# Optimization experiments

Measured on AMD Instinct MI355X. Metric: run time of the kernel, lower is better.

## Reference

```python
import jax, jax.numpy as jnp
import numpy as np

B, T, D, H, HD, FF = 1024, 128, 128, 4, 32, 512
SCALE = D ** -0.5  # NOTE: original scales by full EMBED_DIM**-0.5, not head_dim
EPS = 1e-5


def setup_inputs() -> dict:
    key = jax.random.key(0)
    ks = jax.random.split(key, 14)
    s = 0.02
    return {
        "x": jax.random.normal(ks[0], (B, T, D), dtype=jnp.float32),
        "ln1_g": jnp.ones((D,), jnp.float32),
        "ln1_b": jnp.zeros((D,), jnp.float32),
        "Wq": jax.random.normal(ks[1], (H, HD, D), jnp.float32) * s,
        "Wk": jax.random.normal(ks[2], (H, HD, D), jnp.float32) * s,
        "Wv": jax.random.normal(ks[3], (H, HD, D), jnp.float32) * s,
        "Wo": jax.random.normal(ks[4], (D, D), jnp.float32) * s,
        "bo": jnp.zeros((D,), jnp.float32),
        "ln2_g": jnp.ones((D,), jnp.float32),
        "ln2_b": jnp.zeros((D,), jnp.float32),
        "W1": jax.random.normal(ks[5], (FF, D), jnp.float32) * s,
        "b1": jnp.zeros((FF,), jnp.float32),
        "W2": jax.random.normal(ks[6], (D, FF), jnp.float32) * s,
        "b2": jnp.zeros((D,), jnp.float32),
    }


def _layer_norm(x, g, b):
    mu = jnp.mean(x, axis=-1, keepdims=True)
    var = jnp.mean(jnp.square(x - mu), axis=-1, keepdims=True)
    return (x - mu) * jax.lax.rsqrt(var + EPS) * g + b


def reference(x, ln1_g, ln1_b, Wq, Wk, Wv, Wo, bo, ln2_g, ln2_b, W1, b1, W2, b2):
    # --- attention sub-block ---
    h = _layer_norm(x, ln1_g, ln1_b)                       # [B,T,D]
    q = jnp.einsum('btd,nhd->bnth', h, Wq)                 # [B,H,T,HD]
    k = jnp.einsum('btd,nhd->bnth', h, Wk)
    v = jnp.einsum('btd,nhd->bnth', h, Wv)
    scores = jnp.einsum('bnth,bnsh->bnts', q, k) * SCALE   # [B,H,T,T]
    causal = jnp.tril(jnp.ones((T, T), dtype=bool))
    scores = jnp.where(causal, scores, -jnp.inf)
    w = jax.nn.softmax(scores, axis=-1)                    # dropout = eval identity
    attn = jnp.einsum('bnts,bnsh->bnth', w, v)             # [B,H,T,HD]
    attn = attn.transpose(0, 2, 1, 3).reshape(B, T, D)     # concat heads
    x = x + attn @ Wo.T + bo
    # --- feed-forward sub-block ---
    h2 = _layer_norm(x, ln2_g, ln2_b)
    ff = jax.nn.relu(h2 @ W1.T + b1) @ W2.T + b2
    return x + ff
```

## Files before the change

### kernel.cpp

```cpp
#include <hip/hip_runtime.h>
#include <hip/hip_bf16.h>


typedef short bf16x8 __attribute__((ext_vector_type(8)));
typedef float f32x4  __attribute__((ext_vector_type(4)));
typedef unsigned short u16;
typedef unsigned int   u32;

#define TT   128
#define DDIM 128
#define FFD  512
#define PIT  136

#define OWQ 0
#define OWK 16384
#define OWV 32768
#define OWO 49152
#define OW1 65536
#define OW2 131072
#define WTOT 196608

#define QSC 0.12751744f

#if defined(__has_builtin)
#if __has_builtin(__builtin_amdgcn_exp2f)
#define EXP2F(x) __builtin_amdgcn_exp2f(x)
#else
#define EXP2F(x) exp2f(x)
#endif
#else
#define EXP2F(x) exp2f(x)
#endif

__device__ __forceinline__ u16 f2b(float f) {
    __hip_bfloat16 h = __float2bfloat16(f);
    return __builtin_bit_cast(u16, h);
}
__device__ __forceinline__ u32 pk2(float x, float y) {
    return (u32)f2b(x) | ((u32)f2b(y) << 16);
}
__device__ __forceinline__ void st_b64(u16* p, u32 lo, u32 hi) {
    uint2 v; v.x = lo; v.y = hi;
    *reinterpret_cast<uint2*>(p) = v;
}
__device__ __forceinline__ bf16x8 ldfrag(const u16* p) {
    return __builtin_bit_cast(bf16x8, *reinterpret_cast<const uint4*>(p));
}
__device__ __forceinline__ f32x4 mfma16(bf16x8 a, bf16x8 b, f32x4 c) {
    return __builtin_amdgcn_mfma_f32_16x16x32_bf16(a, b, c, 0, 0, 0);
}

__device__ __forceinline__ void quad_collect_pk(const u32 (&pkv)[8][2],
                                                bf16x8 (&fr)[4], int lane) {
    const int srcA = (lane & 15) + ((lane & 16) << 1);
    const int srcB = srcA + 16;
    const bool hi = (lane & 32) != 0;
    #pragma unroll
    for (int g = 0; g < 4; g++) {
        u32 D00 = pkv[2*g][0],     D01 = pkv[2*g][1];
        u32 D10 = pkv[2*g + 1][0], D11 = pkv[2*g + 1][1];
        u32 a00 = (u32)__shfl((int)D00, srcA);
        u32 a10 = (u32)__shfl((int)D10, srcA);
        u32 a01 = (u32)__shfl((int)D01, srcA);
        u32 a11 = (u32)__shfl((int)D11, srcA);
        u32 b00 = (u32)__shfl((int)D00, srcB);
        u32 b10 = (u32)__shfl((int)D10, srcB);
        u32 b01 = (u32)__shfl((int)D01, srcB);
        u32 b11 = (u32)__shfl((int)D11, srcB);
        uint4 q;
        q.x = hi ? a10 : a00;
        q.y = hi ? a11 : a01;
        q.z = hi ? b10 : b00;
        q.w = hi ? b11 : b01;
        fr[g] = __builtin_bit_cast(bf16x8, q);
    }
}

__global__ __launch_bounds__(256) void wprep(
    const float* __restrict__ wq, const float* __restrict__ wk,
    const float* __restrict__ wv, const float* __restrict__ wo,
    const float* __restrict__ w1, const float* __restrict__ w2,
    u16* __restrict__ dst)
{
    int i = (blockIdx.x * 256 + threadIdx.x) * 8;
    if (i >= WTOT) return;
    const float* s; int off;
    if      (i < OWK) { s = wq; off = i - OWQ; }
    else if (i < OWV) { s = wk; off = i - OWK; }
    else if (i < OWO) { s = wv; off = i - OWV; }
    else if (i < OW1) { s = wo; off = i - OWO; }
    else if (i < OW2) { s = w1; off = i - OW1; }
    else              { s = w2; off = i - OW2; }
    float4 a = *reinterpret_cast<const float4*>(s + off);
    float4 b = *reinterpret_cast<const float4*>(s + off + 4);
    uint4 o;
    o.x = pk2(a.x, a.y); o.y = pk2(a.z, a.w);
    o.z = pk2(b.x, b.y); o.w = pk2(b.z, b.w);
    *reinterpret_cast<uint4*>(dst + i) = o;
}

__global__ __launch_bounds__(512, 2) void tblock_kernel(
    const float* __restrict__ x,
    const float* __restrict__ ln1g, const float* __restrict__ ln1b,
    const u16*  __restrict__ wbf,
    const float* __restrict__ bo,
    const float* __restrict__ ln2g, const float* __restrict__ ln2b,
    const float* __restrict__ b1,   const float* __restrict__ b2,
    float* __restrict__ out)
{
    __shared__ __align__(16) u16 sm[2 * TT * PIT];
    u16* bufK = sm;
    u16* bufV = sm + TT * PIT;

    const int b    = blockIdx.x;
    const int tid  = threadIdx.x;
    const int w    = tid >> 6;
    const int l    = tid & 63;
    const int lq   = l & 15;
    const int quad = l >> 4;
    const int trow = w * 16 + lq;
    const float* xb = x + (size_t)b * (TT * DDIM);

    const u16* wq = wbf + OWQ;
    const u16* wk = wbf + OWK;
    const u16* wv = wbf + OWV;
    const u16* wo = wbf + OWO;
    const u16* w1 = wbf + OW1;
    const u16* w2 = wbf + OW2;

    bf16x8 hf[4];
    {
        float v[32];
        float s = 0.f, s2 = 0.f;
        #pragma unroll
        for (int ks = 0; ks < 4; ks++) {
            const float* src = xb + trow * DDIM + ks * 32 + quad * 8;
            float4 u0 = *reinterpret_cast<const float4*>(src);
            float4 u1 = *reinterpret_cast<const float4*>(src + 4);
            v[ks*8+0]=u0.x; v[ks*8+1]=u0.y; v[ks*8+2]=u0.z; v[ks*8+3]=u0.w;
            v[ks*8+4]=u1.x; v[ks*8+5]=u1.y; v[ks*8+6]=u1.z; v[ks*8+7]=u1.w;
            s  += u0.x+u0.y+u0.z+u0.w + u1.x+u1.y+u1.z+u1.w;
            s2 += u0.x*u0.x+u0.y*u0.y+u0.z*u0.z+u0.w*u0.w
                + u1.x*u1.x+u1.y*u1.y+u1.z*u1.z+u1.w*u1.w;
        }
        s  += __shfl_xor(s, 16);  s2 += __shfl_xor(s2, 16);
        s  += __shfl_xor(s, 32);  s2 += __shfl_xor(s2, 32);
        float mean = s * (1.f / 128.f);
        float var  = fmaxf(s2 * (1.f / 128.f) - mean * mean, 0.f);
        float rstd = rsqrtf(var + 1e-5f);
        #pragma unroll
        for (int ks = 0; ks < 4; ks++) {
            const float* gp = ln1g + ks * 32 + quad * 8;
            const float* bp = ln1b + ks * 32 + quad * 8;
            float4 g0 = *reinterpret_cast<const float4*>(gp);
            float4 g1 = *reinterpret_cast<const float4*>(gp + 4);
            float4 c0 = *reinterpret_cast<const float4*>(bp);
            float4 c1 = *reinterpret_cast<const float4*>(bp + 4);
            float gg[8] = {g0.x,g0.y,g0.z,g0.w,g1.x,g1.y,g1.z,g1.w};
            float bb[8] = {c0.x,c0.y,c0.z,c0.w,c1.x,c1.y,c1.z,c1.w};
            #pragma unroll
            for (int j = 0; j < 8; j++)
                hf[ks][j] = (short)f2b((v[ks*8+j] - mean) * rstd * gg[j] + bb[j]);
        }
    }

    #pragma unroll
    for (int mt = 0; mt < 8; mt++) {
        f32x4 acc = {0, 0, 0, 0};
        #pragma unroll
        for (int ks = 0; ks < 4; ks++) {
            bf16x8 aw = ldfrag(wk + (mt * 16 + lq) * DDIM + ks * 32 + quad * 8);
            acc = mfma16(aw, hf[ks], acc);
        }
        st_b64(bufK + trow * PIT + mt * 16 + quad * 4,
               pk2(acc[0], acc[1]), pk2(acc[2], acc[3]));
    }
    bf16x8 qf[4];
    {
        u32 qpk[8][2];
        #pragma unroll
        for (int mt = 0; mt < 8; mt++) {
            f32x4 acc = {0, 0, 0, 0};
            #pragma unroll
            for (int ks = 0; ks < 4; ks++) {
                bf16x8 aw = ldfrag(wq + (mt * 16 + lq) * DDIM + ks * 32 + quad * 8);
                acc = mfma16(aw, hf[ks], acc);
            }
            qpk[mt][0] = pk2(acc[0] * QSC, acc[1] * QSC);
            qpk[mt][1] = pk2(acc[2] * QSC, acc[3] * QSC);
        }
        quad_collect_pk(qpk, qf, l);
    }
    #pragma unroll
    for (int mt = 0; mt < 8; mt++) {
        f32x4 acc = {0, 0, 0, 0};
        #pragma unroll
        for (int ks = 0; ks < 4; ks++) {
            bf16x8 av = ldfrag(wv + (mt * 16 + lq) * DDIM + ks * 32 + quad * 8);
            acc = mfma16(av, hf[ks], acc);
        }
        #pragma unroll
        for (int r = 0; r < 4; r++)
            bufV[(mt * 16 + quad * 4 + r) * PIT + trow] = f2b(acc[r]);
    }
    __syncthreads();

    #pragma unroll
    for (int h = 0; h < 4; h++) {
        float p[8][4];
        #pragma unroll
        for (int n = 0; n < 8; n++) {
            bf16x8 ka = ldfrag(bufK + (n * 16 + lq) * PIT + h * 32 + quad * 8);
            f32x4 s4 = mfma16(ka, qf[h], f32x4{0, 0, 0, 0});
            #pragma unroll
            for (int r = 0; r < 4; r++) p[n][r] = s4[r];
        }
        __syncthreads();
        float mx = -3.0e38f;
        #pragma unroll
        for (int n = 0; n < 8; n++) {
            #pragma unroll
            for (int r = 0; r < 4; r++) {
                int sc = n * 16 + quad * 4 + r;
                mx = (sc <= trow) ? fmaxf(mx, p[n][r]) : mx;
            }
        }
        mx = fmaxf(mx, __shfl_xor(mx, 16));
        mx = fmaxf(mx, __shfl_xor(mx, 32));
        float sum = 0.f;
        u32 ppk[8][2];
        #pragma unroll
        for (int n = 0; n < 8; n++) {
            float e0, e1, e2, e3;
            {
                int sc = n * 16 + quad * 4;
                e0 = (sc     <= trow) ? EXP2F(p[n][0] - mx) : 0.f;
                e1 = (sc + 1 <= trow) ? EXP2F(p[n][1] - mx) : 0.f;
                e2 = (sc + 2 <= trow) ? EXP2F(p[n][2] - mx) : 0.f;
                e3 = (sc + 3 <= trow) ? EXP2F(p[n][3] - mx) : 0.f;
            }
            sum += e0 + e1 + e2 + e3;
            ppk[n][0] = pk2(e0, e1);
            ppk[n][1] = pk2(e2, e3);
        }
        sum += __shfl_xor(sum, 16);
        sum += __shfl_xor(sum, 32);
        float inv = 1.f / sum;
        bf16x8 pfr[4];
        quad_collect_pk(ppk, pfr, l);
        f32x4 o0 = {0, 0, 0, 0}, o1 = {0, 0, 0, 0};
        #pragma unroll
        for (int ks = 0; ks < 4; ks++) {
            bf16x8 va0 = ldfrag(bufV + (h * 32 + lq) * PIT + ks * 32 + quad * 8);
            bf16x8 va1 = ldfrag(bufV + (h * 32 + 16 + lq) * PIT + ks * 32 + quad * 8);
            o0 = mfma16(va0, pfr[ks], o0);
            o1 = mfma16(va1, pfr[ks], o1);
        }
        #pragma unroll
        for (int r = 0; r < 4; r++) { o0[r] *= inv; o1[r] *= inv; }
        st_b64(bufK + trow * PIT + h * 32 + quad * 4,
               pk2(o0[0], o0[1]), pk2(o0[2], o0[3]));
        st_b64(bufK + trow * PIT + h * 32 + 16 + quad * 4,
               pk2(o1[0], o1[1]), pk2(o1[2], o1[3]));
    }
    __syncthreads();

    float x1res[8][4];
    {
        bf16x8 woa[4];
        #pragma unroll
        for (int ks = 0; ks < 4; ks++)
            woa[ks] = ldfrag(wo + (w * 16 + lq) * DDIM + ks * 32 + quad * 8);
        const float4 bo4 = *reinterpret_cast<const float4*>(bo + w * 16 + quad * 4);
        #pragma unroll
        for (int m = 0; m < 8; m++) {
            f32x4 acc = {0, 0, 0, 0};
            #pragma unroll
            for (int ks = 0; ks < 4; ks++) {
                bf16x8 ab = ldfrag(bufK + (m * 16 + lq) * PIT + ks * 32 + quad * 8);
                acc = mfma16(woa[ks], ab, acc);
            }
            int t = m * 16 + lq;
            const float4 xv = *reinterpret_cast<const float4*>(xb + t * DDIM + w * 16 + quad * 4);
            float v0 = acc[0] + xv.x + bo4.x;
            float v1 = acc[1] + xv.y + bo4.y;
            float v2 = acc[2] + xv.z + bo4.z;
            float v3 = acc[3] + xv.w + bo4.w;
            x1res[m][0] = v0; x1res[m][1] = v1; x1res[m][2] = v2; x1res[m][3] = v3;
            st_b64(bufV + t * PIT + w * 16 + quad * 4, pk2(v0, v1), pk2(v2, v3));
        }
    }
    __syncthreads();

    {
        const int row = tid >> 2, part = tid & 3;
        const u16* src = bufV + row * PIT + part * 32;
        float v[32];
        float s = 0.f, s2 = 0.f;
        #pragma unroll
        for (int i = 0; i < 4; i++) {
            uint4 u = *reinterpret_cast<const uint4*>(src + i * 8);
            u32 arr[4] = {u.x, u.y, u.z, u.w};
            #pragma unroll
            for (int j = 0; j < 4; j++) {
                float f0 = __uint_as_float((arr[j] & 0xffffu) << 16);
                float f1 = __uint_as_float(arr[j] & 0xffff0000u);
                v[i * 8 + 2 * j] = f0; v[i * 8 + 2 * j + 1] = f1;
                s += f0 + f1; s2 += f0 * f0 + f1 * f1;
            }
        }
        s  += __shfl_xor(s, 1);  s2 += __shfl_xor(s2, 1);
        s  += __shfl_xor(s, 2);  s2 += __shfl_xor(s2, 2);
        float mean = s * (1.f / 128.f);
        float var  = fmaxf(s2 * (1.f / 128.f) - mean * mean, 0.f);
        float rstd = rsqrtf(var + 1e-5f);
        u16* dst = bufK + row * PIT + part * 32;
        #pragma unroll
        for (int i = 0; i < 4; i++) {
            u32 o4[4];
            #pragma unroll
            for (int j = 0; j < 4; j++) {
                int c = part * 32 + i * 8 + 2 * j;
                float r0 = (v[i * 8 + 2 * j]     - mean) * rstd * ln2g[c]     + ln2b[c];
                float r1 = (v[i * 8 + 2 * j + 1] - mean) * rstd * ln2g[c + 1] + ln2b[c + 1];
                o4[j] = (u32)f2b(r0) | ((u32)f2b(r1) << 16);
            }
            uint4 pk; pk.x = o4[0]; pk.y = o4[1]; pk.z = o4[2]; pk.w = o4[3];
            *reinterpret_cast<uint4*>(dst + i * 8) = pk;
        }
    }
    __syncthreads();

    f32x4 oacc[8];
    #pragma unroll
    for (int m = 0; m < 8; m++) oacc[m] = f32x4{0, 0, 0, 0};

    #pragma unroll 1
    for (int fc = 0; fc < 4; fc++) {
        const int fbase = fc * 128;
        bf16x8 w1a[4];
        #pragma unroll
        for (int ks = 0; ks < 4; ks++)
            w1a[ks] = ldfrag(w1 + (fbase + w * 16 + lq) * DDIM + ks * 32 + quad * 8);
        const float4 b14 = *reinterpret_cast<const float4*>(b1 + fbase + w * 16 + quad * 4);
        #pragma unroll
        for (int m = 0; m < 8; m++) {
            f32x4 acc = {0, 0, 0, 0};
            #pragma unroll
            for (int ks = 0; ks < 4; ks++) {
                bf16x8 hb = ldfrag(bufK + (m * 16 + lq) * PIT + ks * 32 + quad * 8);
                acc = mfma16(w1a[ks], hb, acc);
            }
            int t = m * 16 + lq;
            float g0 = fmaxf(acc[0] + b14.x, 0.f);
            float g1 = fmaxf(acc[1] + b14.y, 0.f);
            float g2 = fmaxf(acc[2] + b14.z, 0.f);
            float g3 = fmaxf(acc[3] + b14.w, 0.f);
            st_b64(bufV + t * PIT + w * 16 + quad * 4, pk2(g0, g1), pk2(g2, g3));
        }
        __syncthreads();
        bf16x8 w2a[4];
        #pragma unroll
        for (int ks = 0; ks < 4; ks++)
            w2a[ks] = ldfrag(w2 + (w * 16 + lq) * FFD + fbase + ks * 32 + quad * 8);
        #pragma unroll
        for (int m = 0; m < 8; m++) {
            #pragma unroll
            for (int ks = 0; ks < 4; ks++) {
                bf16x8 gb = ldfrag(bufV + (m * 16 + lq) * PIT + ks * 32 + quad * 8);
                oacc[m] = mfma16(w2a[ks], gb, oacc[m]);
            }
        }
        if (fc < 3) __syncthreads();
    }

    {
        const float4 b24 = *reinterpret_cast<const float4*>(b2 + w * 16 + quad * 4);
        float* ob = out + (size_t)b * (TT * DDIM);
        #pragma unroll
        for (int m = 0; m < 8; m++) {
            int t = m * 16 + lq;
            float4 o;
            o.x = oacc[m][0] + x1res[m][0] + b24.x;
            o.y = oacc[m][1] + x1res[m][1] + b24.y;
            o.z = oacc[m][2] + x1res[m][2] + b24.z;
            o.w = oacc[m][3] + x1res[m][3] + b24.w;
            *reinterpret_cast<float4*>(ob + t * DDIM + w * 16 + quad * 4) = o;
        }
    }
}

extern "C" void kernel_launch(void* const* d_in, const int* in_sizes, int n_in,
                              void* d_out, int out_size, void* d_ws, size_t ws_size,
                              hipStream_t stream) {
    const float* x    = (const float*)d_in[0];
    const float* ln1g = (const float*)d_in[1];
    const float* ln1b = (const float*)d_in[2];
    const float* Wq   = (const float*)d_in[3];
    const float* Wk   = (const float*)d_in[4];
    const float* Wv   = (const float*)d_in[5];
    const float* Wo   = (const float*)d_in[6];
    const float* bo   = (const float*)d_in[7];
    const float* ln2g = (const float*)d_in[8];
    const float* ln2b = (const float*)d_in[9];
    const float* W1   = (const float*)d_in[10];
    const float* b1   = (const float*)d_in[11];
    const float* W2   = (const float*)d_in[12];
    const float* b2   = (const float*)d_in[13];
    float* out = (float*)d_out;
    u16* wbf = (u16*)d_ws;

    wprep<<<dim3((WTOT / 8 + 255) / 256), dim3(256), 0, stream>>>(
        Wq, Wk, Wv, Wo, W1, W2, wbf);

    const int nblocks = in_sizes[0] / (TT * DDIM);
    tblock_kernel<<<dim3(nblocks), dim3(512), 0, stream>>>(
        x, ln1g, ln1b, wbf, bo, ln2g, ln2b, b1, b2, out);
}
```

Baseline: 353.3 us.

## Keep per-row activations in registers through Wo, LN2 and FFN, dropping LDS round-trips

After attention, each wave now keeps its 16 token rows in registers. Those rows feed the output projection, the second layer norm (a cross-lane shuffle reduction) and both FFN matmuls, replacing the shared-memory staging buffers and most of the block-wide barriers. The query scale is folded into Wq during weight prep, and the head loop is no longer unrolled. In exchange, each wave reads the full Wo, W1 and W2 weight fragments from global/L2 memory instead of only its 16-row slice, and register pressure rises.

```diff
diff --git a/kernel.cpp b/kernel.cpp
--- a/kernel.cpp
+++ b/kernel.cpp
@@ -84,8 +84,8 @@
 {
     int i = (blockIdx.x * 256 + threadIdx.x) * 8;
     if (i >= WTOT) return;
-    const float* s; int off;
-    if      (i < OWK) { s = wq; off = i - OWQ; }
+    const float* s; int off; float sc = 1.0f;
+    if      (i < OWK) { s = wq; off = i - OWQ; sc = QSC; }
     else if (i < OWV) { s = wk; off = i - OWK; }
     else if (i < OWO) { s = wv; off = i - OWV; }
     else if (i < OW1) { s = wo; off = i - OWO; }
@@ -94,8 +94,8 @@
     float4 a = *reinterpret_cast<const float4*>(s + off);
     float4 b = *reinterpret_cast<const float4*>(s + off + 4);
     uint4 o;
-    o.x = pk2(a.x, a.y); o.y = pk2(a.z, a.w);
-    o.z = pk2(b.x, b.y); o.w = pk2(b.z, b.w);
+    o.x = pk2(a.x * sc, a.y * sc); o.y = pk2(a.z * sc, a.w * sc);
+    o.z = pk2(b.x * sc, b.y * sc); o.w = pk2(b.z * sc, b.w * sc);
     *reinterpret_cast<uint4*>(dst + i) = o;
 }
 
@@ -168,10 +168,8 @@
     for (int mt = 0; mt < 8; mt++) {
         f32x4 acc = {0, 0, 0, 0};
         #pragma unroll
-        for (int ks = 0; ks < 4; ks++) {
-            bf16x8 aw = ldfrag(wk + (mt * 16 + lq) * DDIM + ks * 32 + quad * 8);
-            acc = mfma16(aw, hf[ks], acc);
-        }
+        for (int ks = 0; ks < 4; ks++)
+            acc = mfma16(ldfrag(wk + (mt * 16 + lq) * DDIM + ks * 32 + quad * 8), hf[ks], acc);
         st_b64(bufK + trow * PIT + mt * 16 + quad * 4,
                pk2(acc[0], acc[1]), pk2(acc[2], acc[3]));
     }
@@ -182,12 +180,10 @@
         for (int mt = 0; mt < 8; mt++) {
             f32x4 acc = {0, 0, 0, 0};
             #pragma unroll
-            for (int ks = 0; ks < 4; ks++) {
-                bf16x8 aw = ldfrag(wq + (mt * 16 + lq) * DDIM + ks * 32 + quad * 8);
-                acc = mfma16(aw, hf[ks], acc);
-            }
-            qpk[mt][0] = pk2(acc[0] * QSC, acc[1] * QSC);
-            qpk[mt][1] = pk2(acc[2] * QSC, acc[3] * QSC);
+            for (int ks = 0; ks < 4; ks++)
+                acc = mfma16(ldfrag(wq + (mt * 16 + lq) * DDIM + ks * 32 + quad * 8), hf[ks], acc);
+            qpk[mt][0] = pk2(acc[0], acc[1]);
+            qpk[mt][1] = pk2(acc[2], acc[3]);
         }
         quad_collect_pk(qpk, qf, l);
     }
@@ -195,17 +191,16 @@
     for (int mt = 0; mt < 8; mt++) {
         f32x4 acc = {0, 0, 0, 0};
         #pragma unroll
-        for (int ks = 0; ks < 4; ks++) {
-            bf16x8 av = ldfrag(wv + (mt * 16 + lq) * DDIM + ks * 32 + quad * 8);
-            acc = mfma16(av, hf[ks], acc);
-        }
+        for (int ks = 0; ks < 4; ks++)
+            acc = mfma16(ldfrag(wv + (mt * 16 + lq) * DDIM + ks * 32 + quad * 8), hf[ks], acc);
         #pragma unroll
         for (int r = 0; r < 4; r++)
             bufV[(mt * 16 + quad * 4 + r) * PIT + trow] = f2b(acc[r]);
     }
     __syncthreads();
 
-    #pragma unroll
+    u32 apk[8][2];
+    #pragma unroll 1
     for (int h = 0; h < 4; h++) {
         float p[8][4];
         #pragma unroll
@@ -215,7 +210,6 @@
             #pragma unroll
             for (int r = 0; r < 4; r++) p[n][r] = s4[r];
         }
-        __syncthreads();
         float mx = -3.0e38f;
         #pragma unroll
         for (int n = 0; n < 8; n++) {
@@ -231,14 +225,11 @@
         u32 ppk[8][2];
         #pragma unroll
         for (int n = 0; n < 8; n++) {
-            float e0, e1, e2, e3;
-            {
-                int sc = n * 16 + quad * 4;
-                e0 = (sc     <= trow) ? EXP2F(p[n][0] - mx) : 0.f;
-                e1 = (sc + 1 <= trow) ? EXP2F(p[n][1] - mx) : 0.f;
-                e2 = (sc + 2 <= trow) ? EXP2F(p[n][2] - mx) : 0.f;
-                e3 = (sc + 3 <= trow) ? EXP2F(p[n][3] - mx) : 0.f;
-            }
+            int sc = n * 16 + quad * 4;
+            float e0 = (sc     <= trow) ? EXP2F(p[n][0] - mx) : 0.f;
+            float e1 = (sc + 1 <= trow) ? EXP2F(p[n][1] - mx) : 0.f;
+            float e2 = (sc + 2 <= trow) ? EXP2F(p[n][2] - mx) : 0.f;
+            float e3 = (sc + 3 <= trow) ? EXP2F(p[n][3] - mx) : 0.f;
             sum += e0 + e1 + e2 + e3;
             ppk[n][0] = pk2(e0, e1);
             ppk[n][1] = pk2(e2, e3);
@@ -256,136 +247,101 @@
             o0 = mfma16(va0, pfr[ks], o0);
             o1 = mfma16(va1, pfr[ks], o1);
         }
-        #pragma unroll
-        for (int r = 0; r < 4; r++) { o0[r] *= inv; o1[r] *= inv; }
-        st_b64(bufK + trow * PIT + h * 32 + quad * 4,
-               pk2(o0[0], o0[1]), pk2(o0[2], o0[3]));
-        st_b64(bufK + trow * PIT + h * 32 + 16 + quad * 4,
-               pk2(o1[0], o1[1]), pk2(o1[2], o1[3]));
-    }
-    __syncthreads();
-
-    float x1res[8][4];
-    {
-        bf16x8 woa[4];
-        #pragma unroll
-        for (int ks = 0; ks < 4; ks++)
-            woa[ks] = ldfrag(wo + (w * 16 + lq) * DDIM + ks * 32 + quad * 8);
-        const float4 bo4 = *reinterpret_cast<const float4*>(bo + w * 16 + quad * 4);
-        #pragma unroll
-        for (int m = 0; m < 8; m++) {
+        apk[2 * h + 0][0] = pk2(o0[0] * inv, o0[1] * inv);
+        apk[2 * h + 0][1] = pk2(o0[2] * inv, o0[3] * inv);
+        apk[2 * h + 1][0] = pk2(o1[0] * inv, o1[1] * inv);
+        apk[2 * h + 1][1] = pk2(o1[2] * inv, o1[3] * inv);
+    }
+
+    f32x4 oacc[8];
+    {
+        bf16x8 af[4];
+        quad_collect_pk(apk, af, l);
+        #pragma unroll
+        for (int mt = 0; mt < 8; mt++) {
             f32x4 acc = {0, 0, 0, 0};
             #pragma unroll
-            for (int ks = 0; ks < 4; ks++) {
-                bf16x8 ab = ldfrag(bufK + (m * 16 + lq) * PIT + ks * 32 + quad * 8);
-                acc = mfma16(woa[ks], ab, acc);
+            for (int ks = 0; ks < 4; ks++)
+                acc = mfma16(ldfrag(wo + (mt * 16 + lq) * DDIM + ks * 32 + quad * 8), af[ks], acc);
+            const float4 xv  = *reinterpret_cast<const float4*>(xb + trow * DDIM + mt * 16 + quad * 4);
+            const float4 bo4 = *reinterpret_cast<const float4*>(bo + mt * 16 + quad * 4);
+            oacc[mt][0] = acc[0] + xv.x + bo4.x;
+            oacc[mt][1] = acc[1] + xv.y + bo4.y;
+            oacc[mt][2] = acc[2] + xv.z + bo4.z;
+            oacc[mt][3] = acc[3] + xv.w + bo4.w;
+        }
+    }
+
+    bf16x8 h2f[4];
+    {
+        float s = 0.f, s2 = 0.f;
+        #pragma unroll
+        for (int mt = 0; mt < 8; mt++) {
+            #pragma unroll
+            for (int r = 0; r < 4; r++) {
+                float v = oacc[mt][r];
+                s += v; s2 += v * v;
             }
-            int t = m * 16 + lq;
-            const float4 xv = *reinterpret_cast<const float4*>(xb + t * DDIM + w * 16 + quad * 4);
-            float v0 = acc[0] + xv.x + bo4.x;
-            float v1 = acc[1] + xv.y + bo4.y;
-            float v2 = acc[2] + xv.z + bo4.z;
-            float v3 = acc[3] + xv.w + bo4.w;
-            x1res[m][0] = v0; x1res[m][1] = v1; x1res[m][2] = v2; x1res[m][3] = v3;
-            st_b64(bufV + t * PIT + w * 16 + quad * 4, pk2(v0, v1), pk2(v2, v3));
-        }
-    }
-    __syncthreads();
-
-    {
-        const int row = tid >> 2, part = tid & 3;
-        const u16* src = bufV + row * PIT + part * 32;
-        float v[32];
-        float s = 0.f, s2 = 0.f;
-        #pragma unroll
-        for (int i = 0; i < 4; i++) {
-            uint4 u = *reinterpret_cast<const uint4*>(src + i * 8);
-            u32 arr[4] = {u.x, u.y, u.z, u.w};
-            #pragma unroll
-            for (int j = 0; j < 4; j++) {
-                float f0 = __uint_as_float((arr[j] & 0xffffu) << 16);
-                float f1 = __uint_as_float(arr[j] & 0xffff0000u);
-                v[i * 8 + 2 * j] = f0; v[i * 8 + 2 * j + 1] = f1;
-                s += f0 + f1; s2 += f0 * f0 + f1 * f1;
-            }
-        }
-        s  += __shfl_xor(s, 1);  s2 += __shfl_xor(s2, 1);
-        s  += __shfl_xor(s, 2);  s2 += __shfl_xor(s2, 2);
+        }
+        s  += __shfl_xor(s, 16);  s2 += __shfl_xor(s2, 16);
+        s  += __shfl_xor(s, 32);  s2 += __shfl_xor(s2, 32);
         float mean = s * (1.f / 128.f);
         float var  = fmaxf(s2 * (1.f / 128.f) - mean * mean, 0.f);
         float rstd = rsqrtf(var + 1e-5f);
-        u16* dst = bufK + row * PIT + part * 32;
-        #pragma unroll
-        for (int i = 0; i < 4; i++) {
-            u32 o4[4];
-            #pragma unroll
-            for (int j = 0; j < 4; j++) {
-                int c = part * 32 + i * 8 + 2 * j;
-                float r0 = (v[i * 8 + 2 * j]     - mean) * rstd * ln2g[c]     + ln2b[c];
-                float r1 = (v[i * 8 + 2 * j + 1] - mean) * rstd * ln2g[c + 1] + ln2b[c + 1];
-                o4[j] = (u32)f2b(r0) | ((u32)f2b(r1) << 16);
-            }
-            uint4 pk; pk.x = o4[0]; pk.y = o4[1]; pk.z = o4[2]; pk.w = o4[3];
-            *reinterpret_cast<uint4*>(dst + i * 8) = pk;
-        }
-    }
-    __syncthreads();
-
-    f32x4 oacc[8];
-    #pragma unroll
-    for (int m = 0; m < 8; m++) oacc[m] = f32x4{0, 0, 0, 0};
+        u32 hpk[8][2];
+        #pragma unroll
+        for (int mt = 0; mt < 8; mt++) {
+            const float4 g4 = *reinterpret_cast<const float4*>(ln2g + mt * 16 + quad * 4);
+            const float4 c4 = *reinterpret_cast<const float4*>(ln2b + mt * 16 + quad * 4);
+            float h0 = (oacc[mt][0] - mean) * rstd * g4.x + c4.x;
+            float h1 = (oacc[mt][1] - mean) * rstd * g4.y + c4.y;
+            float h2 = (oacc[mt][2] - mean) * rstd * g4.z + c4.z;
+            float h3 = (oacc[mt][3] - mean) * rstd * g4.w + c4.w;
+            hpk[mt][0] = pk2(h0, h1);
+            hpk[mt][1] = pk2(h2, h3);
+        }
+        quad_collect_pk(hpk, h2f, l);
+    }
 
     #pragma unroll 1
     for (int fc = 0; fc < 4; fc++) {
         const int fbase = fc * 128;
-        bf16x8 w1a[4];
-        #pragma unroll
-        for (int ks = 0; ks < 4; ks++)
-            w1a[ks] = ldfrag(w1 + (fbase + w * 16 + lq) * DDIM + ks * 32 + quad * 8);
-        const float4 b14 = *reinterpret_cast<const float4*>(b1 + fbase + w * 16 + quad * 4);
-        #pragma unroll
-        for (int m = 0; m < 8; m++) {
+        u32 gpk[8][2];
+        #pragma unroll
+        for (int ft = 0; ft < 8; ft++) {
             f32x4 acc = {0, 0, 0, 0};
             #pragma unroll
-            for (int ks = 0; ks < 4; ks++) {
-                bf16x8 hb = ldfrag(bufK + (m * 16 + lq) * PIT + ks * 32 + quad * 8);
-                acc = mfma16(w1a[ks], hb, acc);
-            }
-            int t = m * 16 + lq;
+            for (int ks = 0; ks < 4; ks++)
+                acc = mfma16(ldfrag(w1 + (fbase + ft * 16 + lq) * DDIM + ks * 32 + quad * 8), h2f[ks], acc);
+            const float4 b14 = *reinterpret_cast<const float4*>(b1 + fbase + ft * 16 + quad * 4);
             float g0 = fmaxf(acc[0] + b14.x, 0.f);
             float g1 = fmaxf(acc[1] + b14.y, 0.f);
             float g2 = fmaxf(acc[2] + b14.z, 0.f);
             float g3 = fmaxf(acc[3] + b14.w, 0.f);
-            st_b64(bufV + t * PIT + w * 16 + quad * 4, pk2(g0, g1), pk2(g2, g3));
-        }
-        __syncthreads();
-        bf16x8 w2a[4];
-        #pragma unroll
-        for (int ks = 0; ks < 4; ks++)
-            w2a[ks] = ldfrag(w2 + (w * 16 + lq) * FFD + fbase + ks * 32 + quad * 8);
-        #pragma unroll
-        for (int m = 0; m < 8; m++) {
-            #pragma unroll
-            for (int ks = 0; ks < 4; ks++) {
-                bf16x8 gb = ldfrag(bufV + (m * 16 + lq) * PIT + ks * 32 + quad * 8);
-                oacc[m] = mfma16(w2a[ks], gb, oacc[m]);
-            }
-        }
-        if (fc < 3) __syncthreads();
-    }
-
-    {
-        const float4 b24 = *reinterpret_cast<const float4*>(b2 + w * 16 + quad * 4);
+            gpk[ft][0] = pk2(g0, g1);
+            gpk[ft][1] = pk2(g2, g3);
+        }
+        bf16x8 gf[4];
+        quad_collect_pk(gpk, gf, l);
+        #pragma unroll
+        for (int dt = 0; dt < 8; dt++) {
+            #pragma unroll
+            for (int ks = 0; ks < 4; ks++)
+                oacc[dt] = mfma16(ldfrag(w2 + (dt * 16 + lq) * FFD + fbase + ks * 32 + quad * 8), gf[ks], oacc[dt]);
+        }
+    }
+
+    {
         float* ob = out + (size_t)b * (TT * DDIM);
         #pragma unroll
-        for (int m = 0; m < 8; m++) {
-            int t = m * 16 + lq;
+        for (int dt = 0; dt < 8; dt++) {
+            const float4 b24 = *reinterpret_cast<const float4*>(b2 + dt * 16 + quad * 4);
             float4 o;
-            o.x = oacc[m][0] + x1res[m][0] + b24.x;
-            o.y = oacc[m][1] + x1res[m][1] + b24.y;
-            o.z = oacc[m][2] + x1res[m][2] + b24.z;
-            o.w = oacc[m][3] + x1res[m][3] + b24.w;
-            *reinterpret_cast<float4*>(ob + t * DDIM + w * 16 + quad * 4) = o;
+            o.x = oacc[dt][0] + b24.x;
+            o.y = oacc[dt][1] + b24.y;
+            o.z = oacc[dt][2] + b24.z;
+            o.w = oacc[dt][3] + b24.w;
+            *reinterpret_cast<float4*>(ob + trow * DDIM + dt * 16 + quad * 4) = o;
         }
     }
 }
```

Measured after the change: 581.8 us. 1.65x slower.
